# Kernel tuning notes

Measured on AMD Instinct MI355X. Metric: run time of the kernel, lower is better.

Reference implementation:

```python
import jax, jax.numpy as jnp
import numpy as np
import math

EMBED_DIM = 2048
NUM_HEADS = 16
DEPTH = 12
HEAD_DIM = EMBED_DIM // NUM_HEADS // 2  # 64
LAMBDA_INIT = 0.8 - 0.6 * math.exp(-0.3 * DEPTH)
EPS = 1e-8


def apply_rope(x):
    # x: (b, s, h, d) -- lucidrains interleaved rotary, freqs_for='lang', theta=10000
    b, s, h, d = x.shape
    inv_freq = 1.0 / (10000.0 ** (jnp.arange(0, d, 2, dtype=jnp.float32) / d))
    t = jnp.arange(s, dtype=jnp.float32)
    freqs = t[:, None] * inv_freq[None, :]           # (s, d/2)
    freqs = jnp.repeat(freqs, 2, axis=-1)            # (s, d) pairwise repeat
    cos = jnp.cos(freqs)[None, :, None, :].astype(x.dtype)
    sin = jnp.sin(freqs)[None, :, None, :].astype(x.dtype)
    x1 = x[..., 0::2]
    x2 = x[..., 1::2]
    rot = jnp.stack([-x2, x1], axis=-1).reshape(x.shape)  # rotate_half, interleaved
    return x * cos + rot * sin


def causal_attn(q, k, v):
    # q,k: (b, s, h, d); v: (b, s, h, e). flash_attn_func default scale = d**-0.5
    b, s, h, d = q.shape
    scale = d ** -0.5
    scores = jnp.einsum('bqhd,bkhd->bhqk', q, k) * scale
    mask = jnp.tril(jnp.ones((s, s), dtype=bool))
    scores = jnp.where(mask[None, None], scores, jnp.finfo(scores.dtype).min)
    p = jax.nn.softmax(scores, axis=-1)
    return jnp.einsum('bhqk,bkhe->bqhe', p, v)


def rms_norm(x, w, b):
    var = jnp.mean(jnp.square(x), axis=-1, keepdims=True)
    return x * jax.lax.rsqrt(var + EPS) * w + b


def setup_inputs() -> dict:
    key = jax.random.key(0)
    ks = jax.random.split(key, 11)
    D = EMBED_DIM
    std = D ** -0.5
    return {
        'x': jax.random.normal(ks[0], (2, 2048, D), dtype=jnp.float32),
        'Wq': jax.random.normal(ks[1], (D, D), dtype=jnp.float32) * std,
        'Wk': jax.random.normal(ks[2], (D, D), dtype=jnp.float32) * std,
        'Wv': jax.random.normal(ks[3], (D, D), dtype=jnp.float32) * std,
        'Wo': jax.random.normal(ks[4], (D, D), dtype=jnp.float32) * std,
        'lambda_q1': jax.random.normal(ks[5], (HEAD_DIM,), dtype=jnp.float32) * 0.1,
        'lambda_k1': jax.random.normal(ks[6], (HEAD_DIM,), dtype=jnp.float32) * 0.1,
        'lambda_q2': jax.random.normal(ks[7], (HEAD_DIM,), dtype=jnp.float32) * 0.1,
        'lambda_k2': jax.random.normal(ks[8], (HEAD_DIM,), dtype=jnp.float32) * 0.1,
        'ln_w': jnp.ones((2 * HEAD_DIM,), dtype=jnp.float32),
        'ln_b': jnp.zeros((2 * HEAD_DIM,), dtype=jnp.float32),
    }


def reference(x, Wq, Wk, Wv, Wo, lambda_q1, lambda_k1, lambda_q2, lambda_k2, ln_w, ln_b):
    b, s, D = x.shape
    H, hd = NUM_HEADS, HEAD_DIM
    q = (x @ Wq).reshape(b, s, 2 * H, hd)
    k = (x @ Wk).reshape(b, s, 2 * H, hd)
    v = (x @ Wv).reshape(b, s, H, 2 * hd)
    q = apply_rope(q)
    k = apply_rope(k)
    q = q.reshape(b, s, H, 2, hd)
    k = k.reshape(b, s, H, 2, hd)
    q1, q2 = q[:, :, :, 0], q[:, :, :, 1]
    k1, k2 = k[:, :, :, 0], k[:, :, :, 1]
    attn1 = causal_attn(q1, k1, v)   # (b, s, H, 2*hd)
    attn2 = causal_attn(q2, k2, v)
    lam1 = jnp.exp(jnp.sum(lambda_q1 * lambda_k1))
    lam2 = jnp.exp(jnp.sum(lambda_q2 * lambda_k2))
    lam = lam1 - lam2 + LAMBDA_INIT
    attn = rms_norm(attn1 - lam * attn2, ln_w, ln_b)
    attn = attn * (1.0 - LAMBDA_INIT)
    attn = attn.reshape(b, s, D)
    return attn @ Wo
```

## Files before the change

### kernel.cpp

```cpp
#include <hip/hip_runtime.h>

typedef unsigned short u16;
typedef unsigned int   u32;
typedef short bf16x8 __attribute__((ext_vector_type(8)));
typedef float f32x4  __attribute__((ext_vector_type(4)));

#define SQ 2048
#define DMODEL 2048
#define NROWS 4096
#define LAMBDA_INIT 0.7836057665316245f
#define OUT_SCALE   0.21639423346837552f

__device__ __forceinline__ float bf2f(u16 u) {
    union { u32 u; float f; } x; x.u = ((u32)u) << 16; return x.f;
}
__device__ __forceinline__ u16 f2bf(float f) {
    union { float f; u32 u; } x; x.f = f;
    u32 r = x.u + 0x7fffu + ((x.u >> 16) & 1u);
    return (u16)(r >> 16);
}

__device__ __forceinline__ void gload_lds16(const void* g, void* l) {
    __builtin_amdgcn_global_load_lds((const __attribute__((address_space(1))) void*)g,
                                     (__attribute__((address_space(3))) void*)l,
                                     16, 0, 0);
}

__global__ __launch_bounds__(256) void transpose_w(const float* __restrict__ W0,
                                                   const float* __restrict__ W1,
                                                   const float* __restrict__ W2,
                                                   const float* __restrict__ W3,
                                                   u16* __restrict__ out) {
    __shared__ float tile[32][33];
    const int z = blockIdx.z;
    const float* W = (z == 0) ? W0 : (z == 1) ? W1 : (z == 2) ? W2 : W3;
    u16* O = out + (size_t)z * DMODEL * DMODEL;
    const int tx = threadIdx.x, ty = threadIdx.y;
    const int bx = blockIdx.x, by = blockIdx.y;
#pragma unroll
    for (int j = 0; j < 4; ++j)
        tile[ty + j * 8][tx] = W[(size_t)(by * 32 + ty + j * 8) * DMODEL + bx * 32 + tx];
    __syncthreads();
#pragma unroll
    for (int j = 0; j < 4; ++j)
        O[(size_t)(bx * 32 + ty + j * 8) * DMODEL + by * 32 + tx] = f2bf(tile[tx][ty + j * 8]);
}

__global__ __launch_bounds__(256) void cvt_x(const float* __restrict__ x, u16* __restrict__ xb) {
    const size_t i = ((size_t)blockIdx.x * 256 + threadIdx.x) * 8;
    float4 a = *(const float4*)(x + i);
    float4 b = *(const float4*)(x + i + 4);
    uint4 o;
    o.x = (u32)f2bf(a.x) | ((u32)f2bf(a.y) << 16);
    o.y = (u32)f2bf(a.z) | ((u32)f2bf(a.w) << 16);
    o.z = (u32)f2bf(b.x) | ((u32)f2bf(b.y) << 16);
    o.w = (u32)f2bf(b.z) | ((u32)f2bf(b.w) << 16);
    *(uint4*)(xb + i) = o;
}

template <bool OUT_BF16>
__global__ __launch_bounds__(256) void gemm_bt(const u16* __restrict__ A,
                                               const u16* __restrict__ Bt0,
                                               void* __restrict__ C0) {
    __shared__ u16 As[128 * 32];
    __shared__ u16 Bs[128 * 32];
    const int tid  = threadIdx.x;
    const int lane = tid & 63, wave = tid >> 6;
    const int wm = wave & 1, wn = wave >> 1;
    const int l15 = lane & 15, quad = lane >> 4;
    const int tm = blockIdx.y * 128, tn = blockIdx.x * 128;
    const u16* Bt = Bt0 + (size_t)blockIdx.z * DMODEL * DMODEL;

    const int r_l = lane >> 2, c_l = lane & 3;

    f32x4 acc[4][4] = {};

    for (int k0 = 0; k0 < DMODEL; k0 += 32) {
#pragma unroll
        for (int c = 0; c < 2; ++c) {
            const int chunk = wave * 2 + c;
            const int row = chunk * 16 + r_l;
            gload_lds16(A  + (size_t)(tm + row) * DMODEL + k0 + c_l * 8, &As[chunk * 512]);
            gload_lds16(Bt + (size_t)(tn + row) * DMODEL + k0 + c_l * 8, &Bs[chunk * 512]);
        }
        __syncthreads();
        bf16x8 af[4], bfr[4];
#pragma unroll
        for (int mb = 0; mb < 4; ++mb)
            af[mb] = *(const bf16x8*)(As + (wm * 64 + mb * 16 + l15) * 32 + quad * 8);
#pragma unroll
        for (int nb = 0; nb < 4; ++nb)
            bfr[nb] = *(const bf16x8*)(Bs + (wn * 64 + nb * 16 + l15) * 32 + quad * 8);
#pragma unroll
        for (int mb = 0; mb < 4; ++mb)
#pragma unroll
            for (int nb = 0; nb < 4; ++nb)
                acc[mb][nb] = __builtin_amdgcn_mfma_f32_16x16x32_bf16(af[mb], bfr[nb], acc[mb][nb], 0, 0, 0);
        __syncthreads();
    }
#pragma unroll
    for (int mb = 0; mb < 4; ++mb)
#pragma unroll
        for (int nb = 0; nb < 4; ++nb)
#pragma unroll
            for (int r = 0; r < 4; ++r) {
                const int row = tm + wm * 64 + mb * 16 + quad * 4 + r;
                const int col = tn + wn * 64 + nb * 16 + l15;
                const float v = acc[mb][nb][r];
                if (OUT_BF16) {
                    u16* C = (u16*)C0 + (size_t)blockIdx.z * NROWS * DMODEL;
                    C[(size_t)row * DMODEL + col] = f2bf(v);
                } else {
                    float* C = (float*)C0;
                    C[(size_t)row * DMODEL + col] = v;
                }
            }
}

__global__ __launch_bounds__(256) void rope_kernel(u16* __restrict__ qw, u16* __restrict__ kw) {
    const int row = blockIdx.x;
    const int spos = row & (SQ - 1);
    u16* buf = blockIdx.y ? kw : qw;
    for (int idx = threadIdx.x; idx < 1024; idx += 256) {
        const int h2 = idx >> 5, i = idx & 31;
        const size_t base = (size_t)row * DMODEL + h2 * 64 + 2 * i;
        const float x1 = bf2f(buf[base]), x2 = bf2f(buf[base + 1]);
        const float f = (float)spos * exp2f(-0.41524101186092034f * (float)i);
        const float c = cosf(f), sn = sinf(f);
        buf[base]     = f2bf(x1 * c - x2 * sn);
        buf[base + 1] = f2bf(x2 * c + x1 * sn);
    }
}

__global__ void lam_kernel(const float* __restrict__ lq1, const float* __restrict__ lk1,
                           const float* __restrict__ lq2, const float* __restrict__ lk2,
                           float* __restrict__ out) {
    const int l = threadIdx.x;
    float v1 = lq1[l] * lk1[l];
    float v2 = lq2[l] * lk2[l];
#pragma unroll
    for (int off = 32; off; off >>= 1) {
        v1 += __shfl_xor(v1, off);
        v2 += __shfl_xor(v2, off);
    }
    if (l == 0) out[0] = __expf(v1) - __expf(v2) + LAMBDA_INIT;
}

__global__ __launch_bounds__(256) void vtrans(const u16* __restrict__ vb, u16* __restrict__ vtg) {
    __shared__ u16 tile[64][72];
    const int bh = blockIdx.z;
    const int b = bh >> 4, h = bh & 15;
    const int s0 = blockIdx.x * 64, d0 = blockIdx.y * 64;
    const size_t rowbase = (size_t)b * SQ;
    const int tid = threadIdx.x;
#pragma unroll
    for (int it = 0; it < 2; ++it) {
        const int slot = it * 256 + tid;
        const int key = slot >> 3, dg = slot & 7;
        *(uint4*)&tile[key][dg * 8] =
            *(const uint4*)(vb + (rowbase + s0 + key) * DMODEL + h * 128 + d0 + dg * 8);
    }
    __syncthreads();
#pragma unroll
    for (int it = 0; it < 2; ++it) {
        const int slot = it * 256 + tid;
        const int d = slot >> 3, kg = slot & 7;
        u16 e[8];
#pragma unroll
        for (int j = 0; j < 8; ++j) e[j] = tile[kg * 8 + j][d];
        uint4 o;
        o.x = (u32)e[0] | ((u32)e[1] << 16);
        o.y = (u32)e[2] | ((u32)e[3] << 16);
        o.z = (u32)e[4] | ((u32)e[5] << 16);
        o.w = (u32)e[6] | ((u32)e[7] << 16);
        *(uint4*)(vtg + ((size_t)bh * 128 + d0 + d) * SQ + s0 + kg * 8) = o;
    }
}

__global__ __launch_bounds__(256) void attn_kernel(const u16* __restrict__ qw,
                                                   const u16* __restrict__ kw,
                                                   const u16* __restrict__ vtg,
                                                   const float* __restrict__ lamp,
                                                   const float* __restrict__ lnw,
                                                   const float* __restrict__ lnb,
                                                   u16* __restrict__ yb) {
    __shared__ u16 Ks[64 * 128];
    __shared__ u16 Vts[128 * 64];
    __shared__ u16 Pls[4][16 * 72];

    const int tid = threadIdx.x, lane = tid & 63, wave = tid >> 6;
    const int l15 = lane & 15, quad = lane >> 4;
    const int bh = blockIdx.y, b = bh >> 4, h = bh & 15;
    const size_t rowbase = (size_t)b * SQ;
    const int coff = h * 128;
    const float lam = lamp[0];

#pragma unroll 1
    for (int s = 0; s < 2; ++s) {
        const int strip = s ? (31 - (int)blockIdx.x) : (int)blockIdx.x;
        const int q0 = strip * 64;
        const int nt = strip + 1;

        bf16x8 qf[2][2];
        {
            const size_t qbase = (rowbase + q0 + wave * 16 + l15) * DMODEL + coff + quad * 8;
#pragma unroll
            for (int hf = 0; hf < 2; ++hf)
#pragma unroll
                for (int ks = 0; ks < 2; ++ks)
                    qf[hf][ks] = *(const bf16x8*)(qw + qbase + hf * 64 + ks * 32);
        }

        f32x4 O[2][8] = {};
        float mm[2][4], ll[2][4];
#pragma unroll
        for (int hf = 0; hf < 2; ++hf)
#pragma unroll
            for (int r = 0; r < 4; ++r) { mm[hf][r] = -1e30f; ll[hf][r] = 0.f; }

        for (int t = 0; t < nt; ++t) {
            const int t0 = t * 64;
            __syncthreads();
#pragma unroll
            for (int it = 0; it < 4; ++it) {
                const int slot = it * 256 + tid;
                {
                    const int key = slot >> 4, cg = slot & 15;
                    const int cgp = cg ^ (key & 7);
                    *(uint4*)&Ks[key * 128 + cgp * 8] =
                        *(const uint4*)(kw + (rowbase + t0 + key) * DMODEL + coff + cg * 8);
                }
                {
                    const int d = slot >> 3, kg = slot & 7;
                    const int kgp = kg ^ (d & 7);
                    *(uint4*)&Vts[d * 64 + kgp * 8] =
                        *(const uint4*)(vtg + ((size_t)bh * 128 + d) * SQ + t0 + kg * 8);
                }
            }
            __syncthreads();
            const bool maskt = (t == nt - 1);

#pragma unroll
            for (int hf = 0; hf < 2; ++hf) {
                f32x4 S[4] = {};
#pragma unroll
                for (int nb = 0; nb < 4; ++nb)
#pragma unroll
                    for (int ks = 0; ks < 2; ++ks) {
                        const int cgp = (hf * 8 + ks * 4 + quad) ^ (l15 & 7);
                        bf16x8 kf = *(const bf16x8*)&Ks[(nb * 16 + l15) * 128 + cgp * 8];
                        S[nb] = __builtin_amdgcn_mfma_f32_16x16x32_bf16(qf[hf][ks], kf, S[nb], 0, 0, 0);
                    }
                float mt[4];
#pragma unroll
                for (int r = 0; r < 4; ++r) mt[r] = -1e30f;
#pragma unroll
                for (int nb = 0; nb < 4; ++nb)
#pragma unroll
                    for (int r = 0; r < 4; ++r) {
                        float sv = S[nb][r] * 0.125f;
                        if (maskt && (nb * 16 + l15 > wave * 16 + quad * 4 + r)) sv = -1e30f;
                        S[nb][r] = sv;
                        mt[r] = fmaxf(mt[r], sv);
                    }
#pragma unroll
                for (int r = 0; r < 4; ++r)
#pragma unroll
                    for (int off = 1; off < 16; off <<= 1)
                        mt[r] = fmaxf(mt[r], __shfl_xor(mt[r], off));
                float alpha[4], ps[4];
#pragma unroll
                for (int r = 0; r < 4; ++r) {
                    const float mn = fmaxf(mm[hf][r], mt[r]);
                    alpha[r] = __expf(mm[hf][r] - mn);
                    mm[hf][r] = mn;
                    ps[r] = 0.f;
                }
#pragma unroll
                for (int nb = 0; nb < 4; ++nb)
#pragma unroll
                    for (int r = 0; r < 4; ++r) {
                        const float p = __expf(S[nb][r] - mm[hf][r]);
                        const u16 pq = f2bf(p);
                        ps[r] += bf2f(pq);
                        Pls[wave][(quad * 4 + r) * 72 + nb * 16 + l15] = pq;
                    }
#pragma unroll
                for (int r = 0; r < 4; ++r) {
#pragma unroll
                    for (int off = 1; off < 16; off <<= 1) ps[r] += __shfl_xor(ps[r], off);
                    ll[hf][r] = ll[hf][r] * alpha[r] + ps[r];
                }
#pragma unroll
                for (int nb = 0; nb < 8; ++nb)
#pragma unroll
                    for (int r = 0; r < 4; ++r) O[hf][nb][r] *= alpha[r];
                bf16x8 pf[2];
#pragma unroll
                for (int ks = 0; ks < 2; ++ks)
                    pf[ks] = *(const bf16x8*)&Pls[wave][l15 * 72 + ks * 32 + quad * 8];
#pragma unroll
                for (int nb = 0; nb < 8; ++nb)
#pragma unroll
                    for (int ks = 0; ks < 2; ++ks) {
                        const int kgp = (ks * 4 + quad) ^ (l15 & 7);
                        bf16x8 vf = *(const bf16x8*)&Vts[(nb * 16 + l15) * 64 + kgp * 8];
                        O[hf][nb] = __builtin_amdgcn_mfma_f32_16x16x32_bf16(pf[ks], vf, O[hf][nb], 0, 0, 0);
                    }
            }
        }

        float inl1[4], inl2[4];
#pragma unroll
        for (int r = 0; r < 4; ++r) { inl1[r] = 1.f / ll[0][r]; inl2[r] = 1.f / ll[1][r]; }
        float vv[8][4], ss[4] = {0.f, 0.f, 0.f, 0.f};
#pragma unroll
        for (int nb = 0; nb < 8; ++nb)
#pragma unroll
            for (int r = 0; r < 4; ++r) {
                const float v = O[0][nb][r] * inl1[r] - lam * O[1][nb][r] * inl2[r];
                vv[nb][r] = v;
                ss[r] += v * v;
            }
#pragma unroll
        for (int r = 0; r < 4; ++r) {
#pragma unroll
            for (int off = 1; off < 16; off <<= 1) ss[r] += __shfl_xor(ss[r], off);
            ss[r] = rsqrtf(ss[r] * (1.f / 128.f) + 1e-8f) * OUT_SCALE;
        }
#pragma unroll
        for (int nb = 0; nb < 8; ++nb) {
            const int d = nb * 16 + l15;
            const float w = lnw[d], bb = lnb[d] * OUT_SCALE;
#pragma unroll
            for (int r = 0; r < 4; ++r) {
                const size_t row = rowbase + q0 + wave * 16 + quad * 4 + r;
                yb[row * DMODEL + coff + d] = f2bf(vv[nb][r] * ss[r] * w + bb);
            }
        }
    }
}

#define WT_OFF   0ull
#define XB_OFF   33554432ull
#define Q_OFF    50331648ull
#define K_OFF    67108864ull
#define V_OFF    83886080ull
#define VT_OFF   100663296ull
#define LAM_OFF  117440512ull
#define WS_NEED  117440768ull

extern "C" void kernel_launch(void* const* d_in, const int* in_sizes, int n_in,
                              void* d_out, int out_size, void* d_ws, size_t ws_size,
                              hipStream_t stream) {
    if (ws_size < WS_NEED) return;
    const float* x   = (const float*)d_in[0];
    const float* Wq  = (const float*)d_in[1];
    const float* Wk  = (const float*)d_in[2];
    const float* Wv  = (const float*)d_in[3];
    const float* Wo  = (const float*)d_in[4];
    const float* lq1 = (const float*)d_in[5];
    const float* lk1 = (const float*)d_in[6];
    const float* lq2 = (const float*)d_in[7];
    const float* lk2 = (const float*)d_in[8];
    const float* lnw = (const float*)d_in[9];
    const float* lnb = (const float*)d_in[10];

    char* ws = (char*)d_ws;
    u16* wt  = (u16*)(ws + WT_OFF);
    u16* xb  = (u16*)(ws + XB_OFF);
    u16* qb  = (u16*)(ws + Q_OFF);
    u16* kb  = (u16*)(ws + K_OFF);
    u16* vb  = (u16*)(ws + V_OFF);
    u16* vtg = (u16*)(ws + VT_OFF);
    float* lam = (float*)(ws + LAM_OFF);
    float* out = (float*)d_out;

    transpose_w<<<dim3(64, 64, 4), dim3(32, 8, 1), 0, stream>>>(Wq, Wk, Wv, Wo, wt);
    cvt_x<<<dim3(4096), dim3(256), 0, stream>>>(x, xb);
    gemm_bt<true><<<dim3(16, 32, 3), dim3(256), 0, stream>>>(xb, wt, qb);
    rope_kernel<<<dim3(4096, 2), dim3(256), 0, stream>>>(qb, kb);
    lam_kernel<<<dim3(1), dim3(64), 0, stream>>>(lq1, lk1, lq2, lk2, lam);
    vtrans<<<dim3(32, 2, 32), dim3(256), 0, stream>>>(vb, vtg);
    attn_kernel<<<dim3(16, 32), dim3(256), 0, stream>>>(qb, kb, vtg, lam, lnw, lnb, xb);
    gemm_bt<false><<<dim3(16, 32, 1), dim3(256), 0, stream>>>(xb, wt + 3ull * DMODEL * DMODEL, out);
}
```

Baseline: 545.7 us.

## Double-buffer K/V tiles with async global-to-LDS loads in attention

```diff
diff --git a/kernel.cpp b/kernel.cpp
--- a/kernel.cpp
+++ b/kernel.cpp
@@ -10,6 +10,7 @@
 #define NROWS 4096
 #define LAMBDA_INIT 0.7836057665316245f
 #define OUT_SCALE   0.21639423346837552f
+#define CSC 0.18033688011112042f
 
 __device__ __forceinline__ float bf2f(u16 u) {
     union { u32 u; float f; } x; x.u = ((u32)u) << 16; return x.f;
@@ -184,20 +185,47 @@
                                                    const float* __restrict__ lnw,
                                                    const float* __restrict__ lnb,
                                                    u16* __restrict__ yb) {
-    __shared__ u16 Ks[64 * 128];
-    __shared__ u16 Vts[128 * 64];
+    __shared__ u16 Ks[2][64 * 128];
+    __shared__ u16 Vts[2][128 * 64];
     __shared__ u16 Pls[4][16 * 72];
 
     const int tid = threadIdx.x, lane = tid & 63, wave = tid >> 6;
     const int l15 = lane & 15, quad = lane >> 4;
-    const int bh = blockIdx.y, b = bh >> 4, h = bh & 15;
+    const int bh = blockIdx.x, b = bh >> 4, h = bh & 15;
+    const int pair = blockIdx.y;
     const size_t rowbase = (size_t)b * SQ;
     const int coff = h * 128;
     const float lam = lamp[0];
+    const int nt0 = pair + 1;
+
+    int kOff[4], vOff[4];
+#pragma unroll
+    for (int i = 0; i < 4; ++i) {
+        const int cK  = wave * 4 + i;
+        const int key = cK * 4 + (lane >> 4);
+        const int cg  = (lane & 15) ^ (key & 7);
+        kOff[i] = key * DMODEL + coff + cg * 8;
+        const int dd  = cK * 8 + (lane >> 3);
+        const int kg  = (lane & 7) ^ (lane >> 3);
+        vOff[i] = dd * SQ + kg * 8;
+    }
+    const size_t kBase = rowbase * DMODEL;
+    const size_t vBase = (size_t)bh * 128 * SQ;
+
+    auto stageKV = [&](int t0, int d) {
+#pragma unroll
+        for (int i = 0; i < 4; ++i) {
+            gload_lds16(kw + kBase + (size_t)t0 * DMODEL + kOff[i], &Ks[d][(wave * 4 + i) * 512]);
+            gload_lds16(vtg + vBase + t0 + vOff[i], &Vts[d][(wave * 4 + i) * 512]);
+        }
+    };
+
+    int g = 0;
+    stageKV(0, 0);
 
 #pragma unroll 1
     for (int s = 0; s < 2; ++s) {
-        const int strip = s ? (31 - (int)blockIdx.x) : (int)blockIdx.x;
+        const int strip = s ? (31 - pair) : pair;
         const int q0 = strip * 64;
         const int nt = strip + 1;
 
@@ -218,26 +246,18 @@
 #pragma unroll
             for (int r = 0; r < 4; ++r) { mm[hf][r] = -1e30f; ll[hf][r] = 0.f; }
 
-        for (int t = 0; t < nt; ++t) {
+        for (int t = 0; t < nt; ++t, ++g) {
             const int t0 = t * 64;
             __syncthreads();
-#pragma unroll
-            for (int it = 0; it < 4; ++it) {
-                const int slot = it * 256 + tid;
-                {
-                    const int key = slot >> 4, cg = slot & 15;
-                    const int cgp = cg ^ (key & 7);
-                    *(uint4*)&Ks[key * 128 + cgp * 8] =
-                        *(const uint4*)(kw + (rowbase + t0 + key) * DMODEL + coff + cg * 8);
-                }
-                {
-                    const int d = slot >> 3, kg = slot & 7;
-                    const int kgp = kg ^ (d & 7);
-                    *(uint4*)&Vts[d * 64 + kgp * 8] =
-                        *(const uint4*)(vtg + ((size_t)bh * 128 + d) * SQ + t0 + kg * 8);
+            {
+                const int gn = g + 1;
+                if (gn < 33) {
+                    const int tn = (gn < nt0) ? gn : gn - nt0;
+                    stageKV(tn * 64, gn & 1);
                 }
             }
-            __syncthreads();
+            const u16* __restrict__ KsB = Ks[g & 1];
+            const u16* __restrict__ VtB = Vts[g & 1];
             const bool maskt = (t == nt - 1);
 
 #pragma unroll
@@ -248,7 +268,7 @@
 #pragma unroll
                     for (int ks = 0; ks < 2; ++ks) {
                         const int cgp = (hf * 8 + ks * 4 + quad) ^ (l15 & 7);
-                        bf16x8 kf = *(const bf16x8*)&Ks[(nb * 16 + l15) * 128 + cgp * 8];
+                        bf16x8 kf = *(const bf16x8*)&KsB[(nb * 16 + l15) * 128 + cgp * 8];
                         S[nb] = __builtin_amdgcn_mfma_f32_16x16x32_bf16(qf[hf][ks], kf, S[nb], 0, 0, 0);
                     }
                 float mt[4];
@@ -258,7 +278,7 @@
                 for (int nb = 0; nb < 4; ++nb)
 #pragma unroll
                     for (int r = 0; r < 4; ++r) {
-                        float sv = S[nb][r] * 0.125f;
+                        float sv = S[nb][r] * CSC;
                         if (maskt && (nb * 16 + l15 > wave * 16 + quad * 4 + r)) sv = -1e30f;
                         S[nb][r] = sv;
                         mt[r] = fmaxf(mt[r], sv);
@@ -272,7 +292,7 @@
 #pragma unroll
                 for (int r = 0; r < 4; ++r) {
                     const float mn = fmaxf(mm[hf][r], mt[r]);
-                    alpha[r] = __expf(mm[hf][r] - mn);
+                    alpha[r] = exp2f(mm[hf][r] - mn);
                     mm[hf][r] = mn;
                     ps[r] = 0.f;
                 }
@@ -280,10 +300,10 @@
                 for (int nb = 0; nb < 4; ++nb)
 #pragma unroll
                     for (int r = 0; r < 4; ++r) {
-                        const float p = __expf(S[nb][r] - mm[hf][r]);
-                        const u16 pq = f2bf(p);
-                        ps[r] += bf2f(pq);
-                        Pls[wave][(quad * 4 + r) * 72 + nb * 16 + l15] = pq;
+                        const float p = exp2f(S[nb][r] - mm[hf][r]);
+                        const u32 pu = __builtin_bit_cast(u32, p);
+                        ps[r] += __builtin_bit_cast(float, pu & 0xffff0000u);
+                        Pls[wave][(quad * 4 + r) * 72 + nb * 16 + l15] = (u16)(pu >> 16);
                     }
 #pragma unroll
                 for (int r = 0; r < 4; ++r) {
@@ -304,7 +324,7 @@
 #pragma unroll
                     for (int ks = 0; ks < 2; ++ks) {
                         const int kgp = (ks * 4 + quad) ^ (l15 & 7);
-                        bf16x8 vf = *(const bf16x8*)&Vts[(nb * 16 + l15) * 64 + kgp * 8];
+                        bf16x8 vf = *(const bf16x8*)&VtB[(nb * 16 + l15) * 64 + kgp * 8];
                         O[hf][nb] = __builtin_amdgcn_mfma_f32_16x16x32_bf16(pf[ks], vf, O[hf][nb], 0, 0, 0);
                     }
             }
@@ -382,6 +402,6 @@
     rope_kernel<<<dim3(4096, 2), dim3(256), 0, stream>>>(qb, kb);
     lam_kernel<<<dim3(1), dim3(64), 0, stream>>>(lq1, lk1, lq2, lk2, lam);
     vtrans<<<dim3(32, 2, 32), dim3(256), 0, stream>>>(vb, vtg);
-    attn_kernel<<<dim3(16, 32), dim3(256), 0, stream>>>(qb, kb, vtg, lam, lnw, lnb, xb);
+    attn_kernel<<<dim3(32, 16), dim3(256), 0, stream>>>(qb, kb, vtg, lam, lnw, lnb, xb);
     gemm_bt<false><<<dim3(16, 32, 1), dim3(256), 0, stream>>>(xb, wt + 3ull * DMODEL * DMODEL, out);
 }
```

After: 560.5 us. 1.03x slower.
